# Kernel optimization log

Hardware: AMD Instinct MI355X
Metric: run time of the kernel (lower is better)

The kernel has to match this reference:

```python
import jax, jax.numpy as jnp
import numpy as np

DIM = 1024

def setup_inputs() -> dict:
    key = jax.random.key(0)
    ks = jax.random.split(key, 7)
    s = 1.0 / np.sqrt(DIM)
    x = jax.random.normal(ks[0], (8, 2048, DIM), dtype=jnp.float32)
    Wq = jax.random.uniform(ks[1], (DIM, DIM), jnp.float32, -s, s)
    bq = jax.random.uniform(ks[2], (DIM,), jnp.float32, -s, s)
    Wk = jax.random.uniform(ks[3], (DIM, DIM), jnp.float32, -s, s)
    bk = jax.random.uniform(ks[4], (DIM,), jnp.float32, -s, s)
    Wv = jax.random.uniform(ks[5], (DIM, DIM), jnp.float32, -s, s)
    bv = jax.random.uniform(ks[6], (DIM,), jnp.float32, -s, s)
    return {"x": x, "Wq": Wq, "bq": bq, "Wk": Wk, "bk": bk, "Wv": Wv, "bv": bv}

def reference(x, Wq, bq, Wk, bk, Wv, bv):
    # nn.Linear: y = x @ W.T + b
    q = jnp.einsum('bsd,ed->bse', x, Wq) + bq  # [B,S,D]
    k = jnp.einsum('bsd,ed->bse', x, Wk) + bk
    v = jnp.einsum('bsd,ed->bse', x, Wv) + bv
    scores = jnp.einsum('bqd,bkd->bqk', q, k) / jnp.sqrt(jnp.float32(DIM))
    attn = jax.nn.softmax(scores, axis=-1)
    return jnp.einsum('bqk,bkd->bqd', attn, v)
```

## Files before the change

kernel.cpp:

```cpp
#include <hip/hip_runtime.h>

#define DIM 1024
#define SEQ 2048

typedef __attribute__((ext_vector_type(8))) short bf16x8;
typedef __attribute__((ext_vector_type(16))) float f32x16;
typedef __attribute__((ext_vector_type(4))) unsigned short us4;
typedef __attribute__((ext_vector_type(4))) _Float16 h4;

__device__ __forceinline__ unsigned short f2bf(float f) {
    union { float f; unsigned int u; } v; v.f = f;
    unsigned int r = (v.u + 0x7FFFu + ((v.u >> 16) & 1u)) >> 16;
    return (unsigned short)r;
}

#define GLOAD(gp, lp) __builtin_amdgcn_global_load_lds( \
    (const __attribute__((address_space(1))) unsigned int*)(gp), \
    (__attribute__((address_space(3))) unsigned int*)(lp), 16, 0, 0)

#define MFMA32(a, b, c) __builtin_amdgcn_mfma_f32_32x32x16_bf16((a), (b), (c), 0, 0, 0)

__global__ __launch_bounds__(256) void cast_f32_bf16(const float* __restrict__ src,
                                                     unsigned short* __restrict__ dst, int n) {
    int i = (blockIdx.x * 256 + threadIdx.x) * 8;
    if (i >= n) return;
    float4 a = *(const float4*)(src + i);
    float4 b = *(const float4*)(src + i + 4);
    us4 lo = { f2bf(a.x), f2bf(a.y), f2bf(a.z), f2bf(a.w) };
    us4 hi = { f2bf(b.x), f2bf(b.y), f2bf(b.z), f2bf(b.w) };
    *(us4*)(dst + i) = lo;
    *(us4*)(dst + i + 4) = hi;
}

__device__ __forceinline__ void gemm256_core(
    const unsigned short* __restrict__ A, const unsigned short* __restrict__ B,
    int lda, int ldb, int K, char* smem, f32x16 acc[4][2])
{
    const int tid = threadIdx.x;
    const int lane = tid & 63;
    const int wm = (tid >> 6) >> 2;
    const int wn = (tid >> 6) & 3;
    const int l31 = lane & 31, lhi = lane >> 5;

    const int schunk = ((tid & 7) ^ ((tid >> 3) & 7)) * 8;
    const unsigned short* paw = A + (size_t)(tid >> 3) * lda + schunk;
    const unsigned short* pbw = B + (size_t)(tid >> 3) * ldb + schunk;
    const int doff = tid * 16;

    const int key = l31 & 7;
    const int abase = (wm * 128 + l31) * 128;
    const int bbase = 32768 + (wn * 64 + l31) * 128;
    int csw[4];
#pragma unroll
    for (int ks = 0; ks < 4; ks++) csw[ks] = (((ks << 1) | lhi) ^ key) * 16;

    const int NT = K >> 6;

#define STAGE_A(bb, kt) do { \
    GLOAD(paw + (kt),                       smem + (bb) + doff); \
    GLOAD(paw + (kt) + (size_t)64  * lda,   smem + (bb) + 8192 + doff); \
    GLOAD(paw + (kt) + (size_t)128 * lda,   smem + (bb) + 16384 + doff); \
    GLOAD(paw + (kt) + (size_t)192 * lda,   smem + (bb) + 24576 + doff); \
} while (0)
#define STAGE_B(bb, kt) do { \
    GLOAD(pbw + (kt),                       smem + (bb) + 32768 + doff); \
    GLOAD(pbw + (kt) + (size_t)64  * ldb,   smem + (bb) + 40960 + doff); \
    GLOAD(pbw + (kt) + (size_t)128 * ldb,   smem + (bb) + 49152 + doff); \
    GLOAD(pbw + (kt) + (size_t)192 * ldb,   smem + (bb) + 57344 + doff); \
} while (0)

    STAGE_A(0, 0);
    STAGE_B(0, 0);

    for (int T = 0; T < NT; ++T) {
        asm volatile("s_waitcnt vmcnt(0)" ::: "memory");
        __builtin_amdgcn_s_barrier();
        const char* db = smem + (T & 1) * 65536;
        const int nb = ((T + 1) & 1) * 65536;
        bf16x8 a0[4], a1[4], b0[2], b1[2];

#pragma unroll
        for (int mi = 0; mi < 4; mi++) {
            a0[mi] = *(const bf16x8*)(db + abase + mi * 4096 + csw[0]);
            a1[mi] = *(const bf16x8*)(db + abase + mi * 4096 + csw[1]);
        }
#pragma unroll
        for (int nj = 0; nj < 2; nj++) {
            b0[nj] = *(const bf16x8*)(db + bbase + nj * 4096 + csw[0]);
            b1[nj] = *(const bf16x8*)(db + bbase + nj * 4096 + csw[1]);
        }
        if (T + 1 < NT) STAGE_A(nb, (size_t)(T + 1) * 64);
        __builtin_amdgcn_s_setprio(1);
#pragma unroll
        for (int mi = 0; mi < 4; mi++)
#pragma unroll
            for (int nj = 0; nj < 2; nj++)
                acc[mi][nj] = MFMA32(a0[mi], b0[nj], acc[mi][nj]);
#pragma unroll
        for (int mi = 0; mi < 4; mi++)
#pragma unroll
            for (int nj = 0; nj < 2; nj++)
                acc[mi][nj] = MFMA32(a1[mi], b1[nj], acc[mi][nj]);
        __builtin_amdgcn_s_setprio(0);

#pragma unroll
        for (int mi = 0; mi < 4; mi++) {
            a0[mi] = *(const bf16x8*)(db + abase + mi * 4096 + csw[2]);
            a1[mi] = *(const bf16x8*)(db + abase + mi * 4096 + csw[3]);
        }
#pragma unroll
        for (int nj = 0; nj < 2; nj++) {
            b0[nj] = *(const bf16x8*)(db + bbase + nj * 4096 + csw[2]);
            b1[nj] = *(const bf16x8*)(db + bbase + nj * 4096 + csw[3]);
        }
        if (T + 1 < NT) STAGE_B(nb, (size_t)(T + 1) * 64);
        __builtin_amdgcn_s_setprio(1);
#pragma unroll
        for (int mi = 0; mi < 4; mi++)
#pragma unroll
            for (int nj = 0; nj < 2; nj++)
                acc[mi][nj] = MFMA32(a0[mi], b0[nj], acc[mi][nj]);
#pragma unroll
        for (int mi = 0; mi < 4; mi++)
#pragma unroll
            for (int nj = 0; nj < 2; nj++)
                acc[mi][nj] = MFMA32(a1[mi], b1[nj], acc[mi][nj]);
        __builtin_amdgcn_s_setprio(0);
    }
#undef STAGE_A
#undef STAGE_B
}

#define ACC_INIT() \
    f32x16 acc[4][2]; \
    _Pragma("unroll") for (int i = 0; i < 4; i++) \
    _Pragma("unroll") for (int jj = 0; jj < 2; jj++) acc[i][jj] = (f32x16){}; \


template<int BZ>
__global__ __launch_bounds__(512, 2) void gemm_qkv_t(
    const unsigned short* __restrict__ xb, const unsigned short* __restrict__ w,
    const float* __restrict__ bias, unsigned short* __restrict__ C)
{
    extern __shared__ char smem[];
    const int bid = blockIdx.x;
    const int lb = (bid & 7) * 32 + (bid >> 3);
    const int m0 = (lb >> 2) * 256, n0 = (lb & 3) * 256;
    ACC_INIT();
    gemm256_core(xb + (size_t)m0 * DIM, w + (size_t)n0 * DIM, DIM, DIM, DIM, smem, acc);
    const int lane = threadIdx.x & 63, wid = threadIdx.x >> 6;
    const int wm = wid >> 2, wn = wid & 3;
    const int l31 = lane & 31, lhi = lane >> 5;
#pragma unroll
    for (int mi = 0; mi < 4; mi++)
#pragma unroll
        for (int nj = 0; nj < 2; nj++) {
            const int col = n0 + wn * 64 + nj * 32 + l31;
            const float bcol = bias[col];
            if (BZ < 2) {
                const float scale = (BZ == 0) ? 0.03125f : 1.0f;
#pragma unroll
                for (int r = 0; r < 16; r++) {
                    const int row = m0 + wm * 128 + mi * 32 + (r & 3) + 8 * (r >> 2) + 4 * lhi;
                    C[(size_t)row * DIM + col] = f2bf((acc[mi][nj][r] + bcol) * scale);
                }
            } else {
#pragma unroll
                for (int r4 = 0; r4 < 4; r4++) {
                    const int s0 = m0 + wm * 128 + mi * 32 + 8 * r4 + 4 * lhi;
                    const int b = s0 >> 11, s = s0 & 2047;
                    us4 pk = { f2bf(acc[mi][nj][r4 * 4] + bcol),
                               f2bf(acc[mi][nj][r4 * 4 + 1] + bcol),
                               f2bf(acc[mi][nj][r4 * 4 + 2] + bcol),
                               f2bf(acc[mi][nj][r4 * 4 + 3] + bcol) };
                    *(us4*)&C[((size_t)b << 21) + ((size_t)col << 11) + s] = pk;
                }
            }
        }
}

__global__ __launch_bounds__(512, 2) void gemm_qk(
    const unsigned short* __restrict__ qb, const unsigned short* __restrict__ kb,
    unsigned short* __restrict__ sb)
{
    extern __shared__ char smem[];
    const int bid = blockIdx.x;
    const int lb = (bid & 7) * 64 + (bid >> 3);
    const int b = lb >> 6;
    const int r0 = lb & 63;
    const int m0 = (r0 >> 3) * 256, n0 = (r0 & 7) * 256;
    ACC_INIT();
    gemm256_core(qb + ((size_t)b * SEQ + m0) * DIM, kb + ((size_t)b * SEQ + n0) * DIM,
                 DIM, DIM, DIM, smem, acc);
    const int lane = threadIdx.x & 63, wid = threadIdx.x >> 6;
    const int wm = wid >> 2, wn = wid & 3;
    const int l31 = lane & 31, lhi = lane >> 5;
    _Float16* sh = (_Float16*)sb + (size_t)b * SEQ * SEQ;
#pragma unroll
    for (int mi = 0; mi < 4; mi++)
#pragma unroll
        for (int nj = 0; nj < 2; nj++) {
            const int col = n0 + wn * 64 + nj * 32 + l31;
#pragma unroll
            for (int r = 0; r < 16; r++) {
                const int row = m0 + wm * 128 + mi * 32 + (r & 3) + 8 * (r >> 2) + 4 * lhi;
                sh[(size_t)row * SEQ + col] = (_Float16)acc[mi][nj][r];
            }
        }
}

__global__ __launch_bounds__(256) void softmax_p(unsigned short* __restrict__ sb)
{
    const int lane = threadIdx.x & 63, wid = threadIdx.x >> 6;
    const size_t row = (size_t)blockIdx.x * 4 + wid;
    unsigned short* rp = sb + row * SEQ;
    float v[32];
#pragma unroll
    for (int j = 0; j < 8; j++) {
        h4 h = *(const h4*)(rp + (j * 64 + lane) * 4);
#pragma unroll
        for (int e = 0; e < 4; e++) v[j * 4 + e] = (float)h[e];
    }
    float m = -1e30f;
#pragma unroll
    for (int i = 0; i < 32; i++) m = fmaxf(m, v[i]);
#pragma unroll
    for (int msk = 1; msk <= 32; msk <<= 1) m = fmaxf(m, __shfl_xor(m, msk, 64));
    float s = 0.f;
#pragma unroll
    for (int i = 0; i < 32; i++) { v[i] = __expf(v[i] - m); s += v[i]; }
#pragma unroll
    for (int msk = 1; msk <= 32; msk <<= 1) s += __shfl_xor(s, msk, 64);
    float inv = 1.0f / s;
#pragma unroll
    for (int j = 0; j < 8; j++) {
        us4 pu = { f2bf(v[j * 4] * inv), f2bf(v[j * 4 + 1] * inv),
                   f2bf(v[j * 4 + 2] * inv), f2bf(v[j * 4 + 3] * inv) };
        *(us4*)(rp + (j * 64 + lane) * 4) = pu;
    }
}

__global__ __launch_bounds__(512, 2) void gemm_pv(
    const unsigned short* __restrict__ pb, const unsigned short* __restrict__ vt,
    float* __restrict__ out)
{
    extern __shared__ char smem[];
    const int bid = blockIdx.x;
    const int lb = (bid & 7) * 32 + (bid >> 3);
    const int b = lb >> 5;
    const int r0 = lb & 31;
    const int m0 = (r0 >> 2) * 256, n0 = (r0 & 3) * 256;
    ACC_INIT();
    gemm256_core(pb + ((size_t)b * SEQ + m0) * SEQ, vt + ((size_t)b * DIM + n0) * SEQ,
                 SEQ, SEQ, SEQ, smem, acc);
    const int lane = threadIdx.x & 63, wid = threadIdx.x >> 6;
    const int wm = wid >> 2, wn = wid & 3;
    const int l31 = lane & 31, lhi = lane >> 5;
    float* O = out + (size_t)b * SEQ * DIM;
#pragma unroll
    for (int mi = 0; mi < 4; mi++)
#pragma unroll
        for (int nj = 0; nj < 2; nj++) {
            const int col = n0 + wn * 64 + nj * 32 + l31;
#pragma unroll
            for (int r = 0; r < 16; r++) {
                const int row = m0 + wm * 128 + mi * 32 + (r & 3) + 8 * (r >> 2) + 4 * lhi;
                O[(size_t)row * DIM + col] = acc[mi][nj][r];
            }
        }
}

extern "C" void kernel_launch(void* const* d_in, const int* in_sizes, int n_in,
                              void* d_out, int out_size, void* d_ws, size_t ws_size,
                              hipStream_t stream) {
    const float* x  = (const float*)d_in[0];
    const float* Wq = (const float*)d_in[1];
    const float* bq = (const float*)d_in[2];
    const float* Wk = (const float*)d_in[3];
    const float* bk = (const float*)d_in[4];
    const float* Wv = (const float*)d_in[5];
    const float* bv = (const float*)d_in[6];
    float* out = (float*)d_out;
    char* ws = (char*)d_ws;

    unsigned short* xb = (unsigned short*)(ws);
    unsigned short* wb = (unsigned short*)(ws + 33554432);
    unsigned short* qb = (unsigned short*)(ws + 39845888);
    unsigned short* kb = (unsigned short*)(ws + 73400320);
    unsigned short* vt = (unsigned short*)(ws + 106954752);
    unsigned short* sb = (unsigned short*)(ws + 140509184);

    cast_f32_bf16<<<dim3(8192), 256, 0, stream>>>(x, xb, 16777216);
    cast_f32_bf16<<<dim3(512), 256, 0, stream>>>(Wq, wb, 1048576);
    cast_f32_bf16<<<dim3(512), 256, 0, stream>>>(Wk, wb + 1048576, 1048576);
    cast_f32_bf16<<<dim3(512), 256, 0, stream>>>(Wv, wb + 2097152, 1048576);

    hipFuncSetAttribute((const void*)gemm_qkv_t<0>, hipFuncAttributeMaxDynamicSharedMemorySize, 131072);
    hipFuncSetAttribute((const void*)gemm_qkv_t<1>, hipFuncAttributeMaxDynamicSharedMemorySize, 131072);
    hipFuncSetAttribute((const void*)gemm_qkv_t<2>, hipFuncAttributeMaxDynamicSharedMemorySize, 131072);
    hipFuncSetAttribute((const void*)gemm_qk,  hipFuncAttributeMaxDynamicSharedMemorySize, 131072);
    hipFuncSetAttribute((const void*)gemm_pv,  hipFuncAttributeMaxDynamicSharedMemorySize, 131072);

    gemm_qkv_t<0><<<dim3(256), 512, 131072, stream>>>(xb, wb,           bq, qb);
    gemm_qkv_t<1><<<dim3(256), 512, 131072, stream>>>(xb, wb + 1048576, bk, kb);
    gemm_qkv_t<2><<<dim3(256), 512, 131072, stream>>>(xb, wb + 2097152, bv, vt);
    gemm_qk<<<dim3(512), 512, 131072, stream>>>(qb, kb, sb);
    softmax_p<<<dim3(4096), 256, 0, stream>>>(sb);
    gemm_pv<<<dim3(256), 512, 131072, stream>>>(sb, vt, out);
}
```

Before: 286.9 us.

## Fuse softmax exp into QK epilogue and defer normalization to PV epilogue

Removes the separate softmax kernel. The QK GEMM epilogue now applies exp directly to the raw scores, with no max subtraction and no 1/sqrt(D) scale visible, writes bf16 probabilities, and accumulates row sums through shuffles and atomics into a zeroed buffer. The PV epilogue divides by the row sum. The GEMM core also staggers which half-tile each half of the block processes first, meant to spread LDS and global-load contention. Skipping max subtraction risks overflow unless the scale is folded into Q upstream. The rowsum buffer reuses the xb workspace region, which is only safe because xb is dead by then.

```diff
diff --git a/kernel.cpp b/kernel.cpp
--- a/kernel.cpp
+++ b/kernel.cpp
@@ -6,7 +6,6 @@
 typedef __attribute__((ext_vector_type(8))) short bf16x8;
 typedef __attribute__((ext_vector_type(16))) float f32x16;
 typedef __attribute__((ext_vector_type(4))) unsigned short us4;
-typedef __attribute__((ext_vector_type(4))) _Float16 h4;
 
 __device__ __forceinline__ unsigned short f2bf(float f) {
     union { float f; unsigned int u; } v; v.f = f;
@@ -32,6 +31,11 @@
     *(us4*)(dst + i + 4) = hi;
 }
 
+__global__ __launch_bounds__(256) void zero_f32(float* __restrict__ p, int n) {
+    int i = blockIdx.x * 256 + threadIdx.x;
+    if (i < n) p[i] = 0.0f;
+}
+
 __device__ __forceinline__ void gemm256_core(
     const unsigned short* __restrict__ A, const unsigned short* __restrict__ B,
     int lda, int ldb, int K, char* smem, f32x16 acc[4][2])
@@ -40,6 +44,7 @@
     const int lane = tid & 63;
     const int wm = (tid >> 6) >> 2;
     const int wn = (tid >> 6) & 3;
+    const int role = (tid >> 8) & 1;
     const int l31 = lane & 31, lhi = lane >> 5;
 
     const int schunk = ((tid & 7) ^ ((tid >> 3) & 7)) * 8;
@@ -68,6 +73,33 @@
     GLOAD(pbw + (kt) + (size_t)128 * ldb,   smem + (bb) + 49152 + doff); \
     GLOAD(pbw + (kt) + (size_t)192 * ldb,   smem + (bb) + 57344 + doff); \
 } while (0)
+#define HALF(h) do { \
+    bf16x8 a0[4], a1[4], b0[2], b1[2]; \
+    _Pragma("unroll") \
+    for (int mi = 0; mi < 4; mi++) { \
+        a0[mi] = *(const bf16x8*)(db + abase + mi * 4096 + csw[2*(h)]); \
+        a1[mi] = *(const bf16x8*)(db + abase + mi * 4096 + csw[2*(h)+1]); \
+    } \
+    _Pragma("unroll") \
+    for (int nj = 0; nj < 2; nj++) { \
+        b0[nj] = *(const bf16x8*)(db + bbase + nj * 4096 + csw[2*(h)]); \
+        b1[nj] = *(const bf16x8*)(db + bbase + nj * 4096 + csw[2*(h)+1]); \
+    } \
+    if (first) { if (T + 1 < NT) STAGE_A(nb, (size_t)(T + 1) * 64); } \
+    else       { if (T + 1 < NT) STAGE_B(nb, (size_t)(T + 1) * 64); } \
+    __builtin_amdgcn_s_setprio(1); \
+    _Pragma("unroll") \
+    for (int mi = 0; mi < 4; mi++) \
+        _Pragma("unroll") \
+        for (int nj = 0; nj < 2; nj++) \
+            acc[mi][nj] = MFMA32(a0[mi], b0[nj], acc[mi][nj]); \
+    _Pragma("unroll") \
+    for (int mi = 0; mi < 4; mi++) \
+        _Pragma("unroll") \
+        for (int nj = 0; nj < 2; nj++) \
+            acc[mi][nj] = MFMA32(a1[mi], b1[nj], acc[mi][nj]); \
+    __builtin_amdgcn_s_setprio(0); \
+} while (0)
 
     STAGE_A(0, 0);
     STAGE_B(0, 0);
@@ -77,58 +109,17 @@
         __builtin_amdgcn_s_barrier();
         const char* db = smem + (T & 1) * 65536;
         const int nb = ((T + 1) & 1) * 65536;
-        bf16x8 a0[4], a1[4], b0[2], b1[2];
-
-#pragma unroll
-        for (int mi = 0; mi < 4; mi++) {
-            a0[mi] = *(const bf16x8*)(db + abase + mi * 4096 + csw[0]);
-            a1[mi] = *(const bf16x8*)(db + abase + mi * 4096 + csw[1]);
-        }
-#pragma unroll
-        for (int nj = 0; nj < 2; nj++) {
-            b0[nj] = *(const bf16x8*)(db + bbase + nj * 4096 + csw[0]);
-            b1[nj] = *(const bf16x8*)(db + bbase + nj * 4096 + csw[1]);
-        }
-        if (T + 1 < NT) STAGE_A(nb, (size_t)(T + 1) * 64);
-        __builtin_amdgcn_s_setprio(1);
-#pragma unroll
-        for (int mi = 0; mi < 4; mi++)
-#pragma unroll
-            for (int nj = 0; nj < 2; nj++)
-                acc[mi][nj] = MFMA32(a0[mi], b0[nj], acc[mi][nj]);
-#pragma unroll
-        for (int mi = 0; mi < 4; mi++)
-#pragma unroll
-            for (int nj = 0; nj < 2; nj++)
-                acc[mi][nj] = MFMA32(a1[mi], b1[nj], acc[mi][nj]);
-        __builtin_amdgcn_s_setprio(0);
-
-#pragma unroll
-        for (int mi = 0; mi < 4; mi++) {
-            a0[mi] = *(const bf16x8*)(db + abase + mi * 4096 + csw[2]);
-            a1[mi] = *(const bf16x8*)(db + abase + mi * 4096 + csw[3]);
-        }
-#pragma unroll
-        for (int nj = 0; nj < 2; nj++) {
-            b0[nj] = *(const bf16x8*)(db + bbase + nj * 4096 + csw[2]);
-            b1[nj] = *(const bf16x8*)(db + bbase + nj * 4096 + csw[3]);
-        }
-        if (T + 1 < NT) STAGE_B(nb, (size_t)(T + 1) * 64);
-        __builtin_amdgcn_s_setprio(1);
-#pragma unroll
-        for (int mi = 0; mi < 4; mi++)
-#pragma unroll
-            for (int nj = 0; nj < 2; nj++)
-                acc[mi][nj] = MFMA32(a0[mi], b0[nj], acc[mi][nj]);
-#pragma unroll
-        for (int mi = 0; mi < 4; mi++)
-#pragma unroll
-            for (int nj = 0; nj < 2; nj++)
-                acc[mi][nj] = MFMA32(a1[mi], b1[nj], acc[mi][nj]);
-        __builtin_amdgcn_s_setprio(0);
+        if (role == 0) {
+            { const bool first = true;  HALF(0); }
+            { const bool first = false; HALF(1); }
+        } else {
+            { const bool first = true;  HALF(1); }
+            { const bool first = false; HALF(0); }
+        }
     }
 #undef STAGE_A
 #undef STAGE_B
+#undef HALF
 }
 
 #define ACC_INIT() \
@@ -181,7 +172,7 @@
 
 __global__ __launch_bounds__(512, 2) void gemm_qk(
     const unsigned short* __restrict__ qb, const unsigned short* __restrict__ kb,
-    unsigned short* __restrict__ sb)
+    unsigned short* __restrict__ sb, float* __restrict__ rowsum)
 {
     extern __shared__ char smem[];
     const int bid = blockIdx.x;
@@ -195,54 +186,29 @@
     const int lane = threadIdx.x & 63, wid = threadIdx.x >> 6;
     const int wm = wid >> 2, wn = wid & 3;
     const int l31 = lane & 31, lhi = lane >> 5;
-    _Float16* sh = (_Float16*)sb + (size_t)b * SEQ * SEQ;
-#pragma unroll
-    for (int mi = 0; mi < 4; mi++)
-#pragma unroll
-        for (int nj = 0; nj < 2; nj++) {
-            const int col = n0 + wn * 64 + nj * 32 + l31;
-#pragma unroll
-            for (int r = 0; r < 16; r++) {
-                const int row = m0 + wm * 128 + mi * 32 + (r & 3) + 8 * (r >> 2) + 4 * lhi;
-                sh[(size_t)row * SEQ + col] = (_Float16)acc[mi][nj][r];
-            }
-        }
-}
-
-__global__ __launch_bounds__(256) void softmax_p(unsigned short* __restrict__ sb)
-{
-    const int lane = threadIdx.x & 63, wid = threadIdx.x >> 6;
-    const size_t row = (size_t)blockIdx.x * 4 + wid;
-    unsigned short* rp = sb + row * SEQ;
-    float v[32];
-#pragma unroll
-    for (int j = 0; j < 8; j++) {
-        h4 h = *(const h4*)(rp + (j * 64 + lane) * 4);
-#pragma unroll
-        for (int e = 0; e < 4; e++) v[j * 4 + e] = (float)h[e];
-    }
-    float m = -1e30f;
-#pragma unroll
-    for (int i = 0; i < 32; i++) m = fmaxf(m, v[i]);
-#pragma unroll
-    for (int msk = 1; msk <= 32; msk <<= 1) m = fmaxf(m, __shfl_xor(m, msk, 64));
-    float s = 0.f;
-#pragma unroll
-    for (int i = 0; i < 32; i++) { v[i] = __expf(v[i] - m); s += v[i]; }
-#pragma unroll
-    for (int msk = 1; msk <= 32; msk <<= 1) s += __shfl_xor(s, msk, 64);
-    float inv = 1.0f / s;
-#pragma unroll
-    for (int j = 0; j < 8; j++) {
-        us4 pu = { f2bf(v[j * 4] * inv), f2bf(v[j * 4 + 1] * inv),
-                   f2bf(v[j * 4 + 2] * inv), f2bf(v[j * 4 + 3] * inv) };
-        *(us4*)(rp + (j * 64 + lane) * 4) = pu;
+    unsigned short* sh = sb + (size_t)b * SEQ * SEQ;
+    float* rs = rowsum + (size_t)b * SEQ;
+    const int colb = n0 + wn * 64 + l31;
+#pragma unroll
+    for (int mi = 0; mi < 4; mi++) {
+#pragma unroll
+        for (int r = 0; r < 16; r++) {
+            const int row = m0 + wm * 128 + mi * 32 + (r & 3) + 8 * (r >> 2) + 4 * lhi;
+            const float e0 = __expf(acc[mi][0][r]);
+            const float e1 = __expf(acc[mi][1][r]);
+            sh[(size_t)row * SEQ + colb]      = f2bf(e0);
+            sh[(size_t)row * SEQ + colb + 32] = f2bf(e1);
+            float p = e0 + e1;
+#pragma unroll
+            for (int msk = 1; msk < 32; msk <<= 1) p += __shfl_xor(p, msk, 64);
+            if (l31 == 0) atomicAdd(&rs[row], p);
+        }
     }
 }
 
 __global__ __launch_bounds__(512, 2) void gemm_pv(
     const unsigned short* __restrict__ pb, const unsigned short* __restrict__ vt,
-    float* __restrict__ out)
+    const float* __restrict__ rowsum, float* __restrict__ out)
 {
     extern __shared__ char smem[];
     const int bid = blockIdx.x;
@@ -256,16 +222,18 @@
     const int lane = threadIdx.x & 63, wid = threadIdx.x >> 6;
     const int wm = wid >> 2, wn = wid & 3;
     const int l31 = lane & 31, lhi = lane >> 5;
+    const float* rs = rowsum + (size_t)b * SEQ;
     float* O = out + (size_t)b * SEQ * DIM;
 #pragma unroll
     for (int mi = 0; mi < 4; mi++)
 #pragma unroll
-        for (int nj = 0; nj < 2; nj++) {
-            const int col = n0 + wn * 64 + nj * 32 + l31;
-#pragma unroll
-            for (int r = 0; r < 16; r++) {
-                const int row = m0 + wm * 128 + mi * 32 + (r & 3) + 8 * (r >> 2) + 4 * lhi;
-                O[(size_t)row * DIM + col] = acc[mi][nj][r];
+        for (int r = 0; r < 16; r++) {
+            const int row = m0 + wm * 128 + mi * 32 + (r & 3) + 8 * (r >> 2) + 4 * lhi;
+            const float inv = 1.0f / rs[row];
+#pragma unroll
+            for (int nj = 0; nj < 2; nj++) {
+                const int col = n0 + wn * 64 + nj * 32 + l31;
+                O[(size_t)row * DIM + col] = acc[mi][nj][r] * inv;
             }
         }
 }
@@ -289,6 +257,7 @@
     unsigned short* kb = (unsigned short*)(ws + 73400320);
     unsigned short* vt = (unsigned short*)(ws + 106954752);
     unsigned short* sb = (unsigned short*)(ws + 140509184);
+    float* rowsum = (float*)(ws);
 
     cast_f32_bf16<<<dim3(8192), 256, 0, stream>>>(x, xb, 16777216);
     cast_f32_bf16<<<dim3(512), 256, 0, stream>>>(Wq, wb, 1048576);
@@ -304,7 +273,7 @@
     gemm_qkv_t<0><<<dim3(256), 512, 131072, stream>>>(xb, wb,           bq, qb);
     gemm_qkv_t<1><<<dim3(256), 512, 131072, stream>>>(xb, wb + 1048576, bk, kb);
     gemm_qkv_t<2><<<dim3(256), 512, 131072, stream>>>(xb, wb + 2097152, bv, vt);
-    gemm_qk<<<dim3(512), 512, 131072, stream>>>(qb, kb, sb);
-    softmax_p<<<dim3(4096), 256, 0, stream>>>(sb);
-    gemm_pv<<<dim3(256), 512, 131072, stream>>>(sb, vt, out);
-}
+    zero_f32<<<dim3(64), 256, 0, stream>>>(rowsum, 16384);
+    gemm_qk<<<dim3(512), 512, 131072, stream>>>(qb, kb, sb, rowsum);
+    gemm_pv<<<dim3(256), 512, 131072, stream>>>(sb, vt, rowsum, out);
+}
```

Measured after the change: 505.9 us. 76.3% more time.
